# Optimization experiments

Measured on AMD Instinct MI355X. Metric: run time of the kernel, lower is better.

The kernel has to match this reference:

```python
import jax, jax.numpy as jnp
import numpy as np

CLAMP = 80.0


def setup_inputs() -> dict:
    key = jax.random.key(0)
    ks = jax.random.split(key, 8)
    B, C, D, H, W = 2, 64, 16, 16, 16
    Ck = C // 8  # qk channel dim
    x = jax.random.normal(ks[0], (B, C, D, H, W), dtype=jnp.float32)
    # 1x1x1 Conv3d == pointwise linear over channels
    wq = jax.random.normal(ks[1], (Ck, C), dtype=jnp.float32) * (1.0 / np.sqrt(C))
    bq = jnp.zeros((Ck,), dtype=jnp.float32)
    wk = jax.random.normal(ks[2], (Ck, C), dtype=jnp.float32) * (1.0 / np.sqrt(C))
    bk = jnp.zeros((Ck,), dtype=jnp.float32)
    wv = jax.random.normal(ks[3], (C, C), dtype=jnp.float32) * (1.0 / np.sqrt(C))
    bv = jnp.zeros((C,), dtype=jnp.float32)
    gamma = jnp.zeros((1,), dtype=jnp.float32)
    return {"x": x, "wq": wq, "bq": bq, "wk": wk, "bk": bk,
            "wv": wv, "bv": bv, "gamma": gamma}


def reference(x, wq, bq, wk, bk, wv, bv, gamma):
    B, C, D, H, W = x.shape
    N = D * H * W
    scale = 1.0 / np.sqrt(max(C // 8, 1))
    xf = x.reshape(B, C, N)
    # 1x1 convs as channel matmuls -> [B, Cq, N] / [B, C, N]
    q = jnp.einsum('oc,bcn->bon', wq, xf) + bq[None, :, None]
    k = jnp.einsum('oc,bcn->bon', wk, xf) + bk[None, :, None]
    v = jnp.einsum('oc,bcn->bon', wv, xf) + bv[None, :, None]
    q32, k32, v32 = q.astype(jnp.float32), k.astype(jnp.float32), v.astype(jnp.float32)
    # logits[b,n,m] = sum_o q[b,o,n] k[b,o,m] * scale  (q^T k)
    logits = jnp.einsum('bon,bom->bnm', q32, k32) * scale
    logits = jnp.clip(logits, -CLAMP, CLAMP)
    attn = jax.nn.softmax(logits, axis=-1)  # rows sum to 1
    # out = v @ attn  (note: attn applied on the right, as in source)
    out32 = jnp.einsum('bcn,bnm->bcm', v32, attn)
    out = out32.reshape(B, C, D, H, W).astype(x.dtype)
    return gamma[0] * out + x
```

## Files before the change

### kernel.cpp

```cpp
#include <hip/hip_runtime.h>

#define S2F (0.35355339059327373f * 1.4426950408889634f)

using h2 = decltype(__builtin_amdgcn_cvt_pkrtz(0.0f, 0.0f));
typedef _Float16 half8 __attribute__((ext_vector_type(8)));
typedef float f32x4 __attribute__((ext_vector_type(4)));

static __device__ __forceinline__ h2 u2h(unsigned u) { return __builtin_bit_cast(h2, u); }
static __device__ __forceinline__ unsigned pkf16(float a, float b) {
  return __builtin_bit_cast(unsigned, __builtin_amdgcn_cvt_pkrtz(a, b));
}
static __device__ __forceinline__ half8 u4h8(uint4 u) { return __builtin_bit_cast(half8, u); }


__global__ void __launch_bounds__(256, 4)
qkv_kernel(const float* __restrict__ x,
           const float* __restrict__ wq, const float* __restrict__ bq,
           const float* __restrict__ wk, const float* __restrict__ bk,
           const float* __restrict__ wv, const float* __restrict__ bv,
           unsigned* __restrict__ q4, unsigned* __restrict__ k4,
           unsigned* __restrict__ v16) {
  __shared__ float wls[16][64];
  __shared__ float bias16[16];
  __shared__ float qk_lds[16][32];
  int t = threadIdx.x;
  int bid = blockIdx.x;
  int b = bid / 640;
  int rem = bid - b * 640;
  int tile = rem / 5;
  int type = rem - tile * 5;
  int n0 = tile << 5;
  int j = t & 31, rg = t >> 5;

  float* wflat = &wls[0][0];
  for (int i = t; i < 1024; i += 256) {
    float wv_;
    if (type == 0) wv_ = (i < 512) ? wq[i] : wk[i - 512];
    else           wv_ = wv[((type - 1) << 10) + i];
    wflat[i] = wv_;
  }
  if (t < 16)
    bias16[t] = (type == 0) ? ((t < 8) ? bq[t] : bk[t - 8])
                            : bv[((type - 1) << 4) + t];
  __syncthreads();

  float res0 = bias16[rg * 2], res1 = bias16[rg * 2 + 1];
  const float* xb = x + ((b * 64) << 12) + n0 + j;
  #pragma unroll 1
  for (int c0 = 0; c0 < 64; c0 += 16) {
    float xr[16];
    #pragma unroll
    for (int cc = 0; cc < 16; ++cc) xr[cc] = xb[(c0 + cc) << 12];
    const float4* w0 = (const float4*)&wls[rg * 2][c0];
    const float4* w1 = (const float4*)&wls[rg * 2 + 1][c0];
    #pragma unroll
    for (int c4 = 0; c4 < 4; ++c4) {
      float4 a = w0[c4], bb = w1[c4];
      res0 += a.x * xr[4*c4] + a.y * xr[4*c4+1] + a.z * xr[4*c4+2] + a.w * xr[4*c4+3];
      res1 += bb.x * xr[4*c4] + bb.y * xr[4*c4+1] + bb.z * xr[4*c4+2] + bb.w * xr[4*c4+3];
    }
  }

  if (type == 0) {
    qk_lds[rg * 2][j] = res0;
    qk_lds[rg * 2 + 1][j] = res1;
    __syncthreads();
    if (t < 64) {
      int jj = t & 31;
      bool isq = t < 32;
      int rb = isq ? 0 : 8;
      float sc = isq ? S2F : 1.0f;
      uint4 u;
      u.x = pkf16(sc * qk_lds[rb + 0][jj], sc * qk_lds[rb + 1][jj]);
      u.y = pkf16(sc * qk_lds[rb + 2][jj], sc * qk_lds[rb + 3][jj]);
      u.z = pkf16(sc * qk_lds[rb + 4][jj], sc * qk_lds[rb + 5][jj]);
      u.w = pkf16(sc * qk_lds[rb + 6][jj], sc * qk_lds[rb + 7][jj]);
      unsigned* dst = isq ? q4 : k4;
      *(uint4*)&dst[((b << 12) + n0 + jj) << 2] = u;
    }
  } else {
    int cbase = (type - 1) << 4;
    unsigned nb0 = (unsigned)__builtin_amdgcn_ds_swizzle(
        __builtin_bit_cast(int, res0), 0x041F);
    unsigned nb1 = (unsigned)__builtin_amdgcn_ds_swizzle(
        __builtin_bit_cast(int, res1), 0x041F);
    if (!(j & 1)) {
      int u = j >> 1;
      int up = ((u & 6) << 1) | (((u >> 3) & 1) << 1) | (u & 1);
      int base = (((b << 7) + tile) << 10);
      v16[base + ((cbase + rg * 2) << 4) + up]     = pkf16(res0, __builtin_bit_cast(float, nb0));
      v16[base + ((cbase + rg * 2 + 1) << 4) + up] = pkf16(res1, __builtin_bit_cast(float, nb1));
    }
  }
}

__global__ void __launch_bounds__(256, 4)
rowsum_kernel(const unsigned* __restrict__ q4, const unsigned* __restrict__ k4,
              float* __restrict__ lsv2) {
  __shared__ float ps[8][33];
  int t = threadIdx.x;
  int b = blockIdx.x >> 9;
  int nt0 = (blockIdx.x & 511) << 3;
  int tn = t & 7, tg = t >> 3;
  uint4 qu = *(const uint4*)&q4[((b << 12) + nt0 + tn) << 2];
  h2 q0 = u2h(qu.x), q1 = u2h(qu.y), q2 = u2h(qu.z), q3 = u2h(qu.w);
  float acc = 0.f;
  int m0 = tg << 7;
  #pragma unroll 4
  for (int m = m0; m < m0 + 128; ++m) {
    uint4 ka = *(const uint4*)&k4[((b << 12) + m) << 2];
    float l = __builtin_amdgcn_fdot2(u2h(ka.x), q0, 0.f, false);
    l = __builtin_amdgcn_fdot2(u2h(ka.y), q1, l, false);
    l = __builtin_amdgcn_fdot2(u2h(ka.z), q2, l, false);
    l = __builtin_amdgcn_fdot2(u2h(ka.w), q3, l, false);
    acc += exp2f(l);
  }
  ps[tn][tg] = acc;
  __syncthreads();
  if (t < 8) {
    float s = 0.f;
    #pragma unroll
    for (int j = 0; j < 32; ++j) s += ps[t][j];
    lsv2[(b << 12) + nt0 + t] = -__log2f(s);
  }
}

__global__ void __launch_bounds__(512, 1)
attnout_kernel(const float* __restrict__ x, const unsigned* __restrict__ q4,
               const unsigned* __restrict__ k4, const unsigned* __restrict__ v16,
               const float* __restrict__ lsv2, const float* __restrict__ gamma,
               float* __restrict__ out) {
  __shared__ float red[8][64][36];
  int t = threadIdx.x;
  int b = blockIdx.x >> 7;
  int m0 = (blockIdx.x & 127) << 5;
  int w = t >> 6, l = t & 63;
  int L15 = l & 15, G = l >> 4;

  uint4 bk2[2];
  #pragma unroll
  for (int mh = 0; mh < 2; ++mh) {
    if (l < 16) bk2[mh] = *(const uint4*)&k4[((b << 12) + m0 + mh * 16 + L15) << 2];
    else        bk2[mh] = make_uint4(0, 0, 0, 0);
  }
  f32x4 acc[2][4];
  #pragma unroll
  for (int mh = 0; mh < 2; ++mh)
    #pragma unroll
    for (int cf = 0; cf < 4; ++cf) acc[mh][cf] = (f32x4){0.f, 0.f, 0.f, 0.f};

  const float* svb = lsv2 + (b << 12);
  const unsigned* q4b = q4 + ((long)(b << 12) << 2);
  const unsigned* v16b = v16 + ((long)b << 17);

  auto LOAD = [&](int step, half8& aq0, half8& aq1, f32x4& sv0, f32x4& sv1,
                  uint4* va) {
    int n0 = (w << 9) + (step << 5);
    int nblk = (w << 4) + step;
    aq0 = u4h8(*(const uint4*)&q4b[(n0 + L15) << 2]);
    aq1 = u4h8(*(const uint4*)&q4b[(n0 + 16 + L15) << 2]);
    sv0 = *(const f32x4*)&svb[n0 + (G << 2)];
    sv1 = *(const f32x4*)&svb[n0 + 16 + (G << 2)];
    const unsigned* vblk = v16b + (nblk << 10);
    #pragma unroll
    for (int cf = 0; cf < 4; ++cf)
      va[cf] = *(const uint4*)&vblk[(((cf << 4) + L15) << 4) + (G << 2)];
  };
  auto COMPUTE = [&](half8 aq0, half8 aq1, f32x4 sv0, f32x4 sv1, const uint4* va) {
    #pragma unroll
    for (int mh = 0; mh < 2; ++mh) {
      f32x4 z = {0.f, 0.f, 0.f, 0.f};
      f32x4 d0 = __builtin_amdgcn_mfma_f32_16x16x32_f16(aq0, u4h8(bk2[mh]), z, 0, 0, 0);
      f32x4 d1 = __builtin_amdgcn_mfma_f32_16x16x32_f16(aq1, u4h8(bk2[mh]), z, 0, 0, 0);
      float p0[4], p1[4];
      #pragma unroll
      for (int r = 0; r < 4; ++r) {
        p0[r] = exp2f(d0[r] + sv0[r]);
        p1[r] = exp2f(d1[r] + sv1[r]);
      }
      uint4 Bu;
      Bu.x = pkf16(p0[0], p0[1]);
      Bu.y = pkf16(p0[2], p0[3]);
      Bu.z = pkf16(p1[0], p1[1]);
      Bu.w = pkf16(p1[2], p1[3]);
      half8 Bf = u4h8(Bu);
      #pragma unroll
      for (int cf = 0; cf < 4; ++cf)
        acc[mh][cf] = __builtin_amdgcn_mfma_f32_16x16x32_f16(u4h8(va[cf]), Bf, acc[mh][cf], 0, 0, 0);
    }
  };

  half8 aq0A, aq1A, aq0B, aq1B;
  f32x4 sv0A, sv1A, sv0B, sv1B;
  uint4 vaA[4], vaB[4];
  LOAD(0, aq0A, aq1A, sv0A, sv1A, vaA);
  #pragma unroll 1
  for (int step = 0; step < 16; step += 2) {
    LOAD(step + 1, aq0B, aq1B, sv0B, sv1B, vaB);
    COMPUTE(aq0A, aq1A, sv0A, sv1A, vaA);
    if (step < 14) LOAD(step + 2, aq0A, aq1A, sv0A, sv1A, vaA);
    COMPUTE(aq0B, aq1B, sv0B, sv1B, vaB);
  }

  #pragma unroll
  for (int mh = 0; mh < 2; ++mh)
    #pragma unroll
    for (int cf = 0; cf < 4; ++cf)
      *(f32x4*)&red[w][l][(mh * 4 + cf) * 4] = acc[mh][cf];
  __syncthreads();
  int rl = t & 63, f = t >> 6;
  float g = gamma[0];
  f32x4 s = {0.f, 0.f, 0.f, 0.f};
  #pragma unroll
  for (int ww = 0; ww < 8; ++ww) s += *(const f32x4*)&red[ww][rl][f * 4];
  int mh = f >> 2, cf = f & 3;
  int m = m0 + mh * 16 + (rl & 15);
  int cb = cf * 16 + ((rl >> 4) << 2);
  #pragma unroll
  for (int r = 0; r < 4; ++r) {
    int idx = (((b << 6) + cb + r) << 12) + m;
    out[idx] = g * s[r] + x[idx];
  }
}

extern "C" void kernel_launch(void* const* d_in, const int* in_sizes, int n_in,
                              void* d_out, int out_size, void* d_ws, size_t ws_size,
                              hipStream_t stream) {
  const float* x     = (const float*)d_in[0];
  const float* wq    = (const float*)d_in[1];
  const float* bq    = (const float*)d_in[2];
  const float* wk    = (const float*)d_in[3];
  const float* bk    = (const float*)d_in[4];
  const float* wv    = (const float*)d_in[5];
  const float* bv    = (const float*)d_in[6];
  const float* gamma = (const float*)d_in[7];
  float* out = (float*)d_out;
  unsigned* wsu = (unsigned*)d_ws;
  unsigned* q4  = wsu;
  unsigned* k4  = wsu + 32768;
  unsigned* v16 = wsu + 65536;
  float*    lsv2 = (float*)(wsu + 327680);

  qkv_kernel<<<1280, 256, 0, stream>>>(x, wq, bq, wk, bk, wv, bv, q4, k4, v16);
  rowsum_kernel<<<1024, 256, 0, stream>>>(q4, k4, lsv2);
  attnout_kernel<<<256, 512, 0, stream>>>(x, q4, k4, v16, lsv2, gamma, out);
}
```

Measured before the change: 43.59 us.

## Compute softmax row sums with MFMA instead of scalar fdot2 loop

The rowsum kernel now computes the q·k logits for 32 rows against 16 keys per step with 16x16x32 f16 MFMA instructions (K dim zero-padded from 8 to 32). The exp2 sums are then reduced with lane shuffles and across waves through shared memory. The block shape changes to 512 threads over 256 blocks. The aim is to replace per-thread dot products and repeated global k loads with matrix-core throughput, leaving exp2 as the main cost. The trade-offs are wasted MFMA work on the padding and fewer, larger blocks.

```diff
diff --git a/kernel.cpp b/kernel.cpp
--- a/kernel.cpp
+++ b/kernel.cpp
@@ -94,34 +94,60 @@
   }
 }
 
-__global__ void __launch_bounds__(256, 4)
+__global__ void __launch_bounds__(512, 2)
 rowsum_kernel(const unsigned* __restrict__ q4, const unsigned* __restrict__ k4,
               float* __restrict__ lsv2) {
-  __shared__ float ps[8][33];
+  __shared__ float ps[8][32];
   int t = threadIdx.x;
-  int b = blockIdx.x >> 9;
-  int nt0 = (blockIdx.x & 511) << 3;
-  int tn = t & 7, tg = t >> 3;
-  uint4 qu = *(const uint4*)&q4[((b << 12) + nt0 + tn) << 2];
-  h2 q0 = u2h(qu.x), q1 = u2h(qu.y), q2 = u2h(qu.z), q3 = u2h(qu.w);
-  float acc = 0.f;
-  int m0 = tg << 7;
+  int b = blockIdx.x >> 7;
+  int n0 = (blockIdx.x & 127) << 5;
+  int w = t >> 6, l = t & 63;
+  int L15 = l & 15, G = l >> 4;
+
+  const unsigned* q4b = q4 + ((long)(b << 12) << 2);
+  const unsigned* k4b = k4 + ((long)(b << 12) << 2);
+
+  half8 aq0 = u4h8(*(const uint4*)&q4b[(n0 + L15) << 2]);
+  half8 aq1 = u4h8(*(const uint4*)&q4b[(n0 + 16 + L15) << 2]);
+
+  f32x4 acc0 = {0.f, 0.f, 0.f, 0.f}, acc1 = {0.f, 0.f, 0.f, 0.f};
   #pragma unroll 4
-  for (int m = m0; m < m0 + 128; ++m) {
-    uint4 ka = *(const uint4*)&k4[((b << 12) + m) << 2];
-    float l = __builtin_amdgcn_fdot2(u2h(ka.x), q0, 0.f, false);
-    l = __builtin_amdgcn_fdot2(u2h(ka.y), q1, l, false);
-    l = __builtin_amdgcn_fdot2(u2h(ka.z), q2, l, false);
-    l = __builtin_amdgcn_fdot2(u2h(ka.w), q3, l, false);
-    acc += exp2f(l);
-  }
-  ps[tn][tg] = acc;
+  for (int s = 0; s < 32; ++s) {
+    int m0 = (w << 9) + (s << 4);
+    uint4 bku = (l < 16) ? *(const uint4*)&k4b[(m0 + L15) << 2]
+                         : make_uint4(0, 0, 0, 0);
+    half8 bk = u4h8(bku);
+    f32x4 z = {0.f, 0.f, 0.f, 0.f};
+    f32x4 d0 = __builtin_amdgcn_mfma_f32_16x16x32_f16(aq0, bk, z, 0, 0, 0);
+    f32x4 d1 = __builtin_amdgcn_mfma_f32_16x16x32_f16(aq1, bk, z, 0, 0, 0);
+    #pragma unroll
+    for (int r = 0; r < 4; ++r) {
+      acc0[r] += exp2f(d0[r]);
+      acc1[r] += exp2f(d1[r]);
+    }
+  }
+  #pragma unroll
+  for (int r = 0; r < 4; ++r) {
+    float a0 = acc0[r], a1 = acc1[r];
+    a0 += __shfl_xor(a0, 1); a0 += __shfl_xor(a0, 2);
+    a0 += __shfl_xor(a0, 4); a0 += __shfl_xor(a0, 8);
+    a1 += __shfl_xor(a1, 1); a1 += __shfl_xor(a1, 2);
+    a1 += __shfl_xor(a1, 4); a1 += __shfl_xor(a1, 8);
+    acc0[r] = a0; acc1[r] = a1;
+  }
+  if (L15 == 0) {
+    #pragma unroll
+    for (int r = 0; r < 4; ++r) {
+      ps[w][(G << 2) + r]      = acc0[r];
+      ps[w][16 + (G << 2) + r] = acc1[r];
+    }
+  }
   __syncthreads();
-  if (t < 8) {
+  if (t < 32) {
     float s = 0.f;
     #pragma unroll
-    for (int j = 0; j < 32; ++j) s += ps[t][j];
-    lsv2[(b << 12) + nt0 + t] = -__log2f(s);
+    for (int ww = 0; ww < 8; ++ww) s += ps[ww][t];
+    lsv2[(b << 12) + n0 + t] = -__log2f(s);
   }
 }
 
@@ -242,6 +268,6 @@
   float*    lsv2 = (float*)(wsu + 327680);
 
   qkv_kernel<<<1280, 256, 0, stream>>>(x, wq, bq, wk, bk, wv, bv, q4, k4, v16);
-  rowsum_kernel<<<1024, 256, 0, stream>>>(q4, k4, lsv2);
+  rowsum_kernel<<<256, 512, 0, stream>>>(q4, k4, lsv2);
   attnout_kernel<<<256, 512, 0, stream>>>(x, q4, k4, v16, lsv2, gamma, out);
 }
```

Result: faster. 40.03 us (median of 2 runs) (-8.2%).
